# Optimization experiments

Measured on AMD Instinct MI355X. Metric: run time of the kernel, lower is better.

Reference implementation:

```python
import jax, jax.numpy as jnp
import numpy as np

N = 50000          # nodes
E = 800000         # edges (avg degree 16)
NODE_IN, NODE_OUT = 64, 96
EDGE_IN, EDGE_OUT = 32, 32
CONV = [192, 192]  # hidden_conv_sizes
LIN = [192]        # hidden_linear_sizes
NUM_CLASSES = 2


def _linear_init(k, fan_in, fan_out):
    s = 1.0 / np.sqrt(fan_in)
    kw, kb = jax.random.split(k)
    W = jax.random.uniform(kw, (fan_in, fan_out), jnp.float32, -s, s)
    b = jax.random.uniform(kb, (fan_out,), jnp.float32, -s, s)
    return W, b


def setup_inputs() -> dict:
    key = jax.random.key(0)
    ks = jax.random.split(key, 10)
    node_feats = jax.random.normal(ks[0], (N, NODE_IN), jnp.float32)
    edge_feats = jax.random.normal(ks[1], (E, EDGE_IN), jnp.float32)
    src = jax.random.randint(ks[2], (E,), 0, N)
    dst = jax.random.randint(ks[3], (E,), 0, N)
    Wn, bn = _linear_init(ks[4], NODE_IN, NODE_OUT)
    We, be = _linear_init(ks[5], EDGE_IN, EDGE_OUT)
    Wc0, bc0 = _linear_init(ks[6], NODE_OUT + EDGE_OUT, CONV[0])
    Wc1, bc1 = _linear_init(ks[7], CONV[0], CONV[1])
    Wl0, bl0 = _linear_init(ks[8], CONV[1], LIN[0])
    Wo, bo = _linear_init(ks[9], LIN[0], NUM_CLASSES)
    return dict(node_feats=node_feats, edge_feats=edge_feats,
                Wn=Wn, bn=bn, We=We, be=be,
                Wc0=Wc0, bc0=bc0, Wc1=Wc1, bc1=bc1,
                Wl0=Wl0, bl0=bl0, Wo=Wo, bo=bo,
                src=src, dst=dst)


def reference(node_feats, edge_feats, Wn, bn, We, be, Wc0, bc0, Wc1, bc1,
              Wl0, bl0, Wo, bo, src, dst):
    ones = jnp.ones((E,), jnp.float32)
    deg_in = jnp.clip(jax.ops.segment_sum(ones, dst, num_segments=N), 1.0)
    deg_out = jnp.clip(jax.ops.segment_sum(ones, src, num_segments=N), 1.0)
    inv_in = jax.lax.rsqrt(deg_in)    # D_in^{-1/2}
    inv_out = jax.lax.rsqrt(deg_out)  # D_out^{-1/2}

    # EdgeLayer: per-edge linear, mean-aggregated onto destination nodes
    eh = edge_feats @ We + be                                   # [E, EDGE_OUT]
    edge_h = jax.nn.relu(
        jax.ops.segment_sum(eh, dst, num_segments=N) / deg_in[:, None])

    # NodeEmbeddingLayer: per-node linear
    node_h = jax.nn.relu(node_feats @ Wn + bn)                  # [N, NODE_OUT]

    h = jnp.concatenate([edge_h, node_h], axis=1)               # [N, EDGE_OUT+NODE_OUT]

    # dgl GraphConv (norm='both'): D_in^{-1/2} A D_out^{-1/2} h W + b
    # dropout is identity in eval mode
    for W, b in ((Wc0, bc0), (Wc1, bc1)):
        msg = (h * inv_out[:, None])[src]                       # [E, d] gather
        agg = jax.ops.segment_sum(msg, dst, num_segments=N) * inv_in[:, None]
        h = jax.nn.relu(agg @ W + b)

    h = jax.nn.relu(h @ Wl0 + bl0)
    return h @ Wo + bo                                          # [N, NUM_CLASSES]
```

## Files before the change

kernel.cpp:

```cpp
#include <hip/hip_runtime.h>

#define NN 50000
#define NE 800000
#define CAP 64

typedef unsigned short u16;
typedef __attribute__((ext_vector_type(8))) short bf8_t;
typedef __attribute__((ext_vector_type(4))) float f4_t;

__device__ __forceinline__ u16 f2b(float f) {
    unsigned u = __float_as_uint(f);
    unsigned r = u + 0x7FFF + ((u >> 16) & 1);
    return (u16)(r >> 16);
}

__global__ void build_k(const int* __restrict__ src, const int* __restrict__ dst,
                        int* __restrict__ cursor_in, int* __restrict__ deg_out,
                        int2* __restrict__ csr, int E) {
    int e = blockIdx.x * 256 + threadIdx.x;
    if (e < E) {
        int s = src[e];
        int d = dst[e];
        int p = atomicAdd(cursor_in + d, 1);
        csr[(d << 6) + p] = make_int2(s, e);
        atomicAdd(deg_out + s, 1);
    }
}

__global__ void make_inv_k(const int* __restrict__ deg_in, const int* __restrict__ deg_out,
                           float* __restrict__ inv_in, float* __restrict__ inv_out,
                           float* __restrict__ inv_mean, float* __restrict__ bcoef, int n) {
    int i = blockIdx.x * 256 + threadIdx.x;
    if (i < n) {
        int d_in = deg_in[i];
        float di = fmaxf((float)d_in, 1.0f);
        float dq = fmaxf((float)deg_out[i], 1.0f);
        inv_in[i]   = 1.0f / sqrtf(di);
        inv_out[i]  = 1.0f / sqrtf(dq);
        inv_mean[i] = 1.0f / di;
        bcoef[i]    = (d_in > 0) ? 1.0f : 0.0f;
    }
}

__global__ __launch_bounds__(256) void gather_e2_k(
    const float* __restrict__ ef, const int2* __restrict__ csr,
    const int* __restrict__ deg, float* __restrict__ efa) {
    const int lane = threadIdx.x & 63;
    const int node = __builtin_amdgcn_readfirstlane(blockIdx.x * 4 + (threadIdx.x >> 6));
    const int beg = node << 6;
    const int cnt = deg[node];
    const int off = lane & 31;
    const int half = lane >> 5;
    float acc = 0.0f;

    const int np = cnt >> 1;
    const int nb = np >> 3, rem = np & 7;
    int idx[8];
    if (nb > 0) {
#pragma unroll
        for (int j = 0; j < 8; ++j) idx[j] = csr[beg + 2 * j + half].y;
    }
    for (int b = 0; b < nb; ++b) {
        float lv[8];
#pragma unroll
        for (int j = 0; j < 8; ++j) lv[j] = ef[(size_t)idx[j] * 32 + off];
        int nidx[8];
        const int nbase = beg + 2 * (b + 1) * 8;
        if (b + 1 < nb) {
#pragma unroll
            for (int j = 0; j < 8; ++j) nidx[j] = csr[nbase + 2 * j + half].y;
        }
#pragma unroll
        for (int j = 0; j < 8; ++j) acc += lv[j];
        if (b + 1 < nb) {
#pragma unroll
            for (int j = 0; j < 8; ++j) idx[j] = nidx[j];
        }
    }
    const int tbase = beg + 2 * nb * 8;
    for (int t = 0; t < rem; ++t) acc += ef[(size_t)csr[tbase + 2 * t + half].y * 32 + off];
    if ((cnt & 1) && half == 0) acc += ef[(size_t)csr[beg + cnt - 1].y * 32 + off];

    acc += __shfl_down(acc, 32);
    if (lane < 32) efa[(size_t)node * 32 + off] = acc;
}

template <int D, int LPT>
__global__ __launch_bounds__(256) void gather_b2_k(
    const u16* __restrict__ h, const int2* __restrict__ csr,
    const int* __restrict__ deg, const float* __restrict__ inv_in,
    u16* __restrict__ agg) {
    constexpr int ACT = D / LPT;
    constexpr int NW = LPT / 2;
    const int lane = threadIdx.x & 63;
    const int node = __builtin_amdgcn_readfirstlane(blockIdx.x * 4 + (threadIdx.x >> 6));
    const int beg = node << 6;
    const int cnt = deg[node];
    const int off = (lane < ACT ? lane : ACT - 1) * LPT;

    float acc[LPT];
#pragma unroll
    for (int j = 0; j < LPT; ++j) acc[j] = 0.0f;

    const int nb = cnt >> 4;
    int idx[16];
    if (nb > 0) {
#pragma unroll
        for (int j = 0; j < 16; ++j) idx[j] = csr[beg + j].x;
    }
    for (int b = 0; b < nb; ++b) {
        unsigned lv[16][NW];
#pragma unroll
        for (int j = 0; j < 16; ++j) {
            const unsigned* p = (const unsigned*)(h + (size_t)idx[j] * D + off);
            if constexpr (NW == 2) {
                uint2 t = *(const uint2*)p;
                lv[j][0] = t.x; lv[j][1] = t.y;
            } else {
                lv[j][0] = *p;
            }
        }
        int nidx[16];
        const int nbase = beg + (b + 1) * 16;
        if (b + 1 < nb) {
#pragma unroll
            for (int j = 0; j < 16; ++j) nidx[j] = csr[nbase + j].x;
        }
#pragma unroll
        for (int j = 0; j < 16; ++j)
#pragma unroll
            for (int q = 0; q < NW; ++q) {
                unsigned u = lv[j][q];
                acc[2 * q]     += __uint_as_float(u << 16);
                acc[2 * q + 1] += __uint_as_float(u & 0xffff0000u);
            }
        if (b + 1 < nb) {
#pragma unroll
            for (int j = 0; j < 16; ++j) idx[j] = nidx[j];
        }
    }

    int tb = beg + (nb << 4);
    int rem = cnt & 15;
    if (rem >= 8) {
        int ti[8];
#pragma unroll
        for (int j = 0; j < 8; ++j) ti[j] = csr[tb + j].x;
        unsigned lv[8][NW];
#pragma unroll
        for (int j = 0; j < 8; ++j) {
            const unsigned* p = (const unsigned*)(h + (size_t)ti[j] * D + off);
            if constexpr (NW == 2) {
                uint2 t = *(const uint2*)p;
                lv[j][0] = t.x; lv[j][1] = t.y;
            } else {
                lv[j][0] = *p;
            }
        }
#pragma unroll
        for (int j = 0; j < 8; ++j)
#pragma unroll
            for (int q = 0; q < NW; ++q) {
                unsigned u = lv[j][q];
                acc[2 * q]     += __uint_as_float(u << 16);
                acc[2 * q + 1] += __uint_as_float(u & 0xffff0000u);
            }
        tb += 8;
        rem -= 8;
    }
    for (int t = 0; t < rem; ++t) {
        const unsigned* p = (const unsigned*)(h + (size_t)csr[tb + t].x * D + off);
#pragma unroll
        for (int q = 0; q < NW; ++q) {
            unsigned u = p[q];
            acc[2 * q]     += __uint_as_float(u << 16);
            acc[2 * q + 1] += __uint_as_float(u & 0xffff0000u);
        }
    }

    if (lane < ACT) {
        float sc = inv_in[node];
        unsigned o[NW];
#pragma unroll
        for (int q = 0; q < NW; ++q)
            o[q] = (unsigned)f2b(acc[2 * q] * sc) | ((unsigned)f2b(acc[2 * q + 1] * sc) << 16);
        unsigned* dp = (unsigned*)(agg + (size_t)node * D + off);
        if constexpr (NW == 2) {
            uint2 t; t.x = o[0]; t.y = o[1];
            *(uint2*)dp = t;
        } else {
            *dp = o[0];
        }
    }
}

template <int D_IN, int D_OUT, bool SCALE, bool BROW>
__global__ __launch_bounds__(256) void gemm_tile_k(
    const float* __restrict__ in, int in_stride,
    const float* __restrict__ W, const float* __restrict__ bias,
    const float* __restrict__ scale, const float* __restrict__ brow,
    const float* __restrict__ posts,
    u16* __restrict__ out, int out_stride, int n) {
    constexpr int TMW = 8;
    constexpr int ROWS = TMW * 4;
    constexpr int NOUT = (D_OUT + 63) / 64;
    __shared__ float s_in[ROWS * D_IN];

    const int tid = threadIdx.x;
    const int lane = tid & 63;
    const int wave = tid >> 6;
    const int row0 = blockIdx.x * ROWS;

    constexpr int NV = ROWS * D_IN / 4;
    for (int i = tid; i < NV; i += 256) {
        int m = i / (D_IN / 4);
        int kv = i % (D_IN / 4);
        int row = min(row0 + m, n - 1);
        float4 v = *(const float4*)(in + (size_t)row * in_stride + kv * 4);
        if (SCALE) {
            float s = scale[row];
            v.x *= s; v.y *= s; v.z *= s; v.w *= s;
        }
        *(float4*)(s_in + m * D_IN + kv * 4) = v;
    }
    __syncthreads();

    int f[NOUT], ff[NOUT];
    bool fok[NOUT];
    float bv[NOUT];
#pragma unroll
    for (int o = 0; o < NOUT; ++o) {
        f[o] = lane + 64 * o;
        fok[o] = (f[o] < D_OUT);
        ff[o] = fok[o] ? f[o] : 0;
        bv[o] = bias[ff[o]];
    }

    const float* s_my = s_in + wave * TMW * D_IN;

    float acc[NOUT][TMW];
#pragma unroll
    for (int o = 0; o < NOUT; ++o)
#pragma unroll
        for (int m = 0; m < TMW; ++m) acc[o][m] = 0.0f;

    for (int k = 0; k < D_IN; k += 4) {
        float w[4][NOUT];
#pragma unroll
        for (int j = 0; j < 4; ++j)
#pragma unroll
            for (int o = 0; o < NOUT; ++o) w[j][o] = W[(k + j) * D_OUT + ff[o]];
#pragma unroll
        for (int m = 0; m < TMW; ++m) {
            float4 a = *(const float4*)(s_my + m * D_IN + k);
#pragma unroll
            for (int o = 0; o < NOUT; ++o) {
                acc[o][m] = fmaf(a.x, w[0][o], acc[o][m]);
                acc[o][m] = fmaf(a.y, w[1][o], acc[o][m]);
                acc[o][m] = fmaf(a.z, w[2][o], acc[o][m]);
                acc[o][m] = fmaf(a.w, w[3][o], acc[o][m]);
            }
        }
    }

#pragma unroll
    for (int m = 0; m < TMW; ++m) {
        int row = row0 + wave * TMW + m;
        if (row < n) {
            float bc = BROW ? brow[row] : 1.0f;
            float pm = posts[row];
#pragma unroll
            for (int o = 0; o < NOUT; ++o) {
                if (!fok[o]) continue;
                float v = fmaxf(acc[o][m] + bv[o] * bc, 0.0f) * pm;
                out[(size_t)row * out_stride + f[o]] = f2b(v);
            }
        }
    }
}

template <int K>
__global__ void pack_w_k(const float* __restrict__ W, u16* __restrict__ Wp) {
    constexpr int KS = K / 32;
    int idx = blockIdx.x * 256 + threadIdx.x;
    if (idx >= 12 * KS * 64) return;
    int l = idx & 63;
    int s = (idx >> 6) % KS;
    int t = (idx >> 6) / KS;
    int col = t * 16 + (l & 15);
    int krow = s * 32 + ((l >> 4) * 8);
    u16 tmp[8] __attribute__((aligned(16)));
#pragma unroll
    for (int j = 0; j < 8; ++j) tmp[j] = f2b(W[(size_t)(krow + j) * 192 + col]);
    *(uint4*)(Wp + (size_t)idx * 8) = *(const uint4*)tmp;
}

template <int K>
__global__ __launch_bounds__(256) void mfma_gemm_k(
    const u16* __restrict__ A, const u16* __restrict__ Wp,
    const float* __restrict__ bias, const float* __restrict__ posts,
    u16* __restrict__ outB, int n) {
    constexpr int KS = K / 32;
    const int tid = threadIdx.x;
    const int lane = tid & 63;
    const int w = tid >> 6;
    const int row0 = blockIdx.x * 16;
    const int arow = row0 + (lane & 15);
    const int kbase = (lane >> 4) * 8;

    f4_t acc[3];
#pragma unroll
    for (int o = 0; o < 3; ++o) acc[o] = (f4_t){0.f, 0.f, 0.f, 0.f};

    const u16* ap = A + (size_t)arow * K + kbase;
#pragma unroll
    for (int s = 0; s < KS; ++s) {
        bf8_t af = *(const bf8_t*)(ap + s * 32);
#pragma unroll
        for (int o = 0; o < 3; ++o) {
            int t = w * 3 + o;
            bf8_t bf = *(const bf8_t*)(Wp + (size_t)((t * KS + s) * 64 + lane) * 8);
            acc[o] = __builtin_amdgcn_mfma_f32_16x16x32_bf16(af, bf, acc[o], 0, 0, 0);
        }
    }

    const int drow = row0 + (lane >> 4) * 4;
    const int dcol = lane & 15;
    float pm[4];
#pragma unroll
    for (int r = 0; r < 4; ++r) pm[r] = posts[drow + r];
#pragma unroll
    for (int o = 0; o < 3; ++o) {
        int col = (w * 3 + o) * 16 + dcol;
        float bv = bias[col];
#pragma unroll
        for (int r = 0; r < 4; ++r) {
            float v = fmaxf(acc[o][r] + bv, 0.0f) * pm[r];
            outB[(size_t)(drow + r) * 192 + col] = f2b(v);
        }
    }
}

__global__ __launch_bounds__(256) void mfma_fused_k(
    const u16* __restrict__ A,
    const u16* __restrict__ Wp1, const float* __restrict__ b1,
    const u16* __restrict__ Wp2, const float* __restrict__ b2,
    const float* __restrict__ Wo, const float* __restrict__ bo,
    float* __restrict__ out, int n) {
    constexpr int KS = 6;
    constexpr int S = 200;
    __shared__ float sbuf[16 * S];
    __shared__ float s_head[16][17][2];

    const int tid = threadIdx.x;
    const int lane = tid & 63;
    const int w = tid >> 6;
    const int row0 = blockIdx.x * 16;
    const int arow = row0 + (lane & 15);
    const int kbase = (lane >> 4) * 8;
    const int drow = (lane >> 4) * 4;
    const int dcol = lane & 15;

    f4_t acc[3];
#pragma unroll
    for (int o = 0; o < 3; ++o) acc[o] = (f4_t){0.f, 0.f, 0.f, 0.f};

    const u16* ap = A + (size_t)arow * 192 + kbase;
#pragma unroll
    for (int s = 0; s < KS; ++s) {
        bf8_t af = *(const bf8_t*)(ap + s * 32);
#pragma unroll
        for (int o = 0; o < 3; ++o) {
            int t = w * 3 + o;
            bf8_t bf = *(const bf8_t*)(Wp1 + (size_t)((t * KS + s) * 64 + lane) * 8);
            acc[o] = __builtin_amdgcn_mfma_f32_16x16x32_bf16(af, bf, acc[o], 0, 0, 0);
        }
    }

    u16* h2 = (u16*)sbuf;
#pragma unroll
    for (int o = 0; o < 3; ++o) {
        int col = (w * 3 + o) * 16 + dcol;
        float bv = b1[col];
#pragma unroll
        for (int r = 0; r < 4; ++r)
            h2[(drow + r) * S + col] = f2b(fmaxf(acc[o][r] + bv, 0.0f));
    }
    __syncthreads();

#pragma unroll
    for (int o = 0; o < 3; ++o) acc[o] = (f4_t){0.f, 0.f, 0.f, 0.f};
    const u16* hp = h2 + (lane & 15) * S + kbase;
#pragma unroll
    for (int s = 0; s < KS; ++s) {
        bf8_t af = *(const bf8_t*)(hp + s * 32);
#pragma unroll
        for (int o = 0; o < 3; ++o) {
            int t = w * 3 + o;
            bf8_t bf = *(const bf8_t*)(Wp2 + (size_t)((t * KS + s) * 64 + lane) * 8);
            acc[o] = __builtin_amdgcn_mfma_f32_16x16x32_bf16(af, bf, acc[o], 0, 0, 0);
        }
    }
    __syncthreads();

#pragma unroll
    for (int o = 0; o < 3; ++o) {
        int col = (w * 3 + o) * 16 + dcol;
        float bv = b2[col];
#pragma unroll
        for (int r = 0; r < 4; ++r)
            sbuf[(drow + r) * S + col] = fmaxf(acc[o][r] + bv, 0.0f);
    }
    __syncthreads();

    {
        int r = tid >> 4;
        int seg = tid & 15;
        const float* hr = sbuf + r * S + seg * 12;
        const float* wor = Wo + seg * 24;
        float p0 = 0.0f, p1 = 0.0f;
#pragma unroll
        for (int c = 0; c < 12; ++c) {
            float hv = hr[c];
            p0 = fmaf(hv, wor[c * 2 + 0], p0);
            p1 = fmaf(hv, wor[c * 2 + 1], p1);
        }
        s_head[r][seg][0] = p0;
        s_head[r][seg][1] = p1;
    }
    __syncthreads();
    if (tid < 32) {
        int r = tid >> 1, c = tid & 1;
        float sum = bo[c];
#pragma unroll
        for (int g = 0; g < 16; ++g) sum += s_head[r][g][c];
        int row = row0 + r;
        if (row < n) out[(size_t)row * 2 + c] = sum;
    }
}

extern "C" void kernel_launch(void* const* d_in, const int* in_sizes, int n_in,
                              void* d_out, int out_size, void* d_ws, size_t ws_size,
                              hipStream_t stream) {
    const float* node_feats = (const float*)d_in[0];
    const float* edge_feats = (const float*)d_in[1];
    const float* Wn  = (const float*)d_in[2];
    const float* bn  = (const float*)d_in[3];
    const float* We  = (const float*)d_in[4];
    const float* be  = (const float*)d_in[5];
    const float* Wc0 = (const float*)d_in[6];
    const float* bc0 = (const float*)d_in[7];
    const float* Wc1 = (const float*)d_in[8];
    const float* bc1 = (const float*)d_in[9];
    const float* Wl0 = (const float*)d_in[10];
    const float* bl0 = (const float*)d_in[11];
    const float* Wo  = (const float*)d_in[12];
    const float* bo  = (const float*)d_in[13];
    const int* src = (const int*)d_in[14];
    const int* dst = (const int*)d_in[15];
    float* out = (float*)d_out;

    const int N = NN, E = NE;

    int* din       = (int*)d_ws;
    int* dout      = din + N;
    int2* csr      = (int2*)(dout + N);
    float* inv_in   = (float*)(csr + (size_t)CAP * N);
    float* inv_out  = inv_in + N;
    float* inv_mean = inv_out + N;
    float* bcoef    = inv_mean + N;
    float* efa      = bcoef + N;
    u16* h0   = (u16*)(efa + (size_t)32 * N);
    u16* aggA = h0 + (size_t)128 * N;
    u16* h1   = aggA + (size_t)128 * N;
    u16* aggB = h1 + (size_t)192 * N;
    u16* Wp0  = aggB + (size_t)192 * N;
    u16* Wp1  = Wp0 + 128 * 192;
    u16* Wp2  = Wp1 + 192 * 192;

    hipMemsetAsync(d_ws, 0, (size_t)2 * N * sizeof(int), stream);

    const int GB32 = (N + 31) / 32;
    const int GB16 = N / 16;
    const int GW4  = (N + 3) / 4;

    pack_w_k<128><<<dim3(12), dim3(256), 0, stream>>>(Wc0, Wp0);
    pack_w_k<192><<<dim3(18), dim3(256), 0, stream>>>(Wc1, Wp1);
    pack_w_k<192><<<dim3(18), dim3(256), 0, stream>>>(Wl0, Wp2);

    build_k<<<dim3((E + 255) / 256), dim3(256), 0, stream>>>(src, dst, din, dout, csr, E);
    make_inv_k<<<dim3((N + 255) / 256), dim3(256), 0, stream>>>(din, dout, inv_in, inv_out,
                                                                inv_mean, bcoef, N);

    gather_e2_k<<<dim3(GW4), dim3(256), 0, stream>>>(edge_feats, csr, din, efa);
    gemm_tile_k<32, 32, true, true><<<dim3(GB32), dim3(256), 0, stream>>>(
        efa, 32, We, be, inv_mean, bcoef, inv_out, h0, 128, N);
    gemm_tile_k<64, 96, false, false><<<dim3(GB32), dim3(256), 0, stream>>>(
        node_feats, 64, Wn, bn, nullptr, nullptr, inv_out, h0 + 32, 128, N);

    gather_b2_k<128, 2><<<dim3(GW4), dim3(256), 0, stream>>>(h0, csr, din, inv_in, aggA);
    mfma_gemm_k<128><<<dim3(GB16), dim3(256), 0, stream>>>(aggA, Wp0, bc0, inv_out, h1, N);

    gather_b2_k<192, 4><<<dim3(GW4), dim3(256), 0, stream>>>(h1, csr, din, inv_in, aggB);
    mfma_fused_k<<<dim3(GB16), dim3(256), 0, stream>>>(aggB, Wp1, bc1, Wp2, bl0, Wo, bo,
                                                       out, N);
}
```

Baseline: 455.8 us.

## Build CSR via two-pass bucketed partition instead of global atomics

Replaces the per-edge global atomic CSR build with a two-stage scheme. Edges are first bucketed by destination block of 128 nodes, using LDS histograms and per-block staging. A second kernel then fills the per-node CSR slots using LDS atomics and writes the in-degree. This cuts contended global atomics and scattered writes, but adds an extra pass through a temporary buffer aliased onto h1. It also packs src and dst into 16 bits each, which truncates node ids of 65536 or more (N=50000 fits), and caps each bucket at 3072 edges, silently dropping any overflow.

```diff
diff --git a/kernel.cpp b/kernel.cpp
--- a/kernel.cpp
+++ b/kernel.cpp
@@ -4,7 +4,14 @@
 #define NE 800000
 #define CAP 64
 
+#define NPB 128
+#define NBKT 391
+#define NBKT_PAD 512
+#define BCAP 3072
+#define CHUNK 4096
+
 typedef unsigned short u16;
+typedef unsigned long long u64;
 typedef __attribute__((ext_vector_type(8))) short bf8_t;
 typedef __attribute__((ext_vector_type(4))) float f4_t;
 
@@ -14,17 +21,102 @@
     return (u16)(r >> 16);
 }
 
-__global__ void build_k(const int* __restrict__ src, const int* __restrict__ dst,
-                        int* __restrict__ cursor_in, int* __restrict__ deg_out,
-                        int2* __restrict__ csr, int E) {
-    int e = blockIdx.x * 256 + threadIdx.x;
-    if (e < E) {
+__global__ __launch_bounds__(256) void partition_k(
+    const int* __restrict__ src, const int* __restrict__ dst,
+    int* __restrict__ deg_out, int* __restrict__ bktc,
+    u64* __restrict__ part, int E) {
+    __shared__ unsigned cnt[NBKT_PAD];
+    __shared__ unsigned base[NBKT_PAD];
+    __shared__ unsigned cur[NBKT_PAD];
+    __shared__ unsigned gbase[NBKT_PAD];
+    __shared__ unsigned wtot[4];
+    __shared__ u64 staged[CHUNK];
+
+    const int tid = threadIdx.x;
+    const int lane = tid & 63;
+    const int wid = tid >> 6;
+    const int e0 = blockIdx.x * CHUNK;
+    const int n = min(CHUNK, E - e0);
+
+    for (int i = tid; i < NBKT_PAD; i += 256) cnt[i] = 0;
+    __syncthreads();
+
+    for (int i = tid; i < n; i += 256) {
+        int d = dst[e0 + i];
+        atomicAdd(&cnt[d >> 7], 1u);
+    }
+    __syncthreads();
+
+    {
+        unsigned a = cnt[2 * tid];
+        unsigned b = cnt[2 * tid + 1];
+        unsigned ps = a + b;
+        unsigned inc = ps;
+#pragma unroll
+        for (int d = 1; d < 64; d <<= 1) {
+            unsigned v = __shfl_up(inc, d);
+            if (lane >= d) inc += v;
+        }
+        if (lane == 63) wtot[wid] = inc;
+        __syncthreads();
+        unsigned wb = 0;
+#pragma unroll
+        for (int k = 0; k < 4; ++k) wb += (k < wid) ? wtot[k] : 0;
+        unsigned eb = wb + inc - ps;
+        base[2 * tid] = eb;
+        base[2 * tid + 1] = eb + a;
+        cur[2 * tid] = eb;
+        cur[2 * tid + 1] = eb + a;
+    }
+    __syncthreads();
+
+    for (int i = tid; i < n; i += 256) {
+        int e = e0 + i;
+        int d = dst[e];
         int s = src[e];
-        int d = dst[e];
-        int p = atomicAdd(cursor_in + d, 1);
-        csr[(d << 6) + p] = make_int2(s, e);
         atomicAdd(deg_out + s, 1);
-    }
+        unsigned p = atomicAdd(&cur[d >> 7], 1u);
+        staged[p] = ((u64)(unsigned)e << 32) | (((unsigned)d << 16) | (unsigned)s);
+    }
+    __syncthreads();
+
+    for (int b = tid; b < NBKT; b += 256) {
+        unsigned c = cur[b] - base[b];
+        if (c) gbase[b] = (unsigned)atomicAdd(&bktc[b], (int)c);
+    }
+    __syncthreads();
+
+    for (int i = tid; i < n; i += 256) {
+        u64 v = staged[i];
+        int b = (int)((v >> 16) & 0xffffu) >> 7;
+        unsigned idx = gbase[b] + ((unsigned)i - base[b]);
+        if (idx < BCAP) part[(size_t)b * BCAP + idx] = v;
+    }
+}
+
+__global__ __launch_bounds__(256) void fill_k(
+    const u64* __restrict__ part, const int* __restrict__ bktc,
+    int2* __restrict__ csr, int* __restrict__ din, int n) {
+    __shared__ unsigned cur[NPB];
+    const int tid = threadIdx.x;
+    const int b = blockIdx.x;
+    const int node0 = b << 7;
+    if (tid < NPB) cur[tid] = 0;
+    __syncthreads();
+
+    const int cnt = min(bktc[b], BCAP);
+    const u64* p = part + (size_t)b * BCAP;
+    for (int i = tid; i < cnt; i += 256) {
+        u64 v = p[i];
+        int s = (int)(v & 0xffffu);
+        int d = (int)((v >> 16) & 0xffffu);
+        int e = (int)(v >> 32);
+        unsigned q = atomicAdd(&cur[d & (NPB - 1)], 1u);
+        if (q < CAP) csr[((size_t)d << 6) + q] = make_int2(s, e);
+    }
+    __syncthreads();
+    int node = node0 + tid;
+    if (tid < NPB && node < n) din[node] = (int)cur[tid];
 }
 
 __global__ void make_inv_k(const int* __restrict__ deg_in, const int* __restrict__ deg_out,
@@ -462,9 +554,10 @@
 
     const int N = NN, E = NE;
 
-    int* din       = (int*)d_ws;
-    int* dout      = din + N;
-    int2* csr      = (int2*)(dout + N);
+    int* dout      = (int*)d_ws;
+    int* bktc      = dout + N;
+    int* din       = bktc + NBKT_PAD;
+    int2* csr      = (int2*)(din + N);
     float* inv_in   = (float*)(csr + (size_t)CAP * N);
     float* inv_out  = inv_in + N;
     float* inv_mean = inv_out + N;
@@ -477,8 +570,9 @@
     u16* Wp0  = aggB + (size_t)192 * N;
     u16* Wp1  = Wp0 + 128 * 192;
     u16* Wp2  = Wp1 + 192 * 192;
-
-    hipMemsetAsync(d_ws, 0, (size_t)2 * N * sizeof(int), stream);
+    u64* part = (u64*)h1;
+
+    hipMemsetAsync(d_ws, 0, (size_t)(N + NBKT_PAD) * sizeof(int), stream);
 
     const int GB32 = (N + 31) / 32;
     const int GB16 = N / 16;
@@ -488,7 +582,9 @@
     pack_w_k<192><<<dim3(18), dim3(256), 0, stream>>>(Wc1, Wp1);
     pack_w_k<192><<<dim3(18), dim3(256), 0, stream>>>(Wl0, Wp2);
 
-    build_k<<<dim3((E + 255) / 256), dim3(256), 0, stream>>>(src, dst, din, dout, csr, E);
+    partition_k<<<dim3((E + CHUNK - 1) / CHUNK), dim3(256), 0, stream>>>(
+        src, dst, dout, bktc, part, E);
+    fill_k<<<dim3(NBKT), dim3(256), 0, stream>>>(part, bktc, csr, din, N);
     make_inv_k<<<dim3((N + 255) / 256), dim3(256), 0, stream>>>(din, dout, inv_in, inv_out,
                                                                 inv_mean, bcoef, N);
 
```

Result: faster. 437.2 us (-4.1%).
